# Performance work log

Hardware: AMD Instinct MI355X
Metric: run time of the kernel (lower is better)

Reference implementation:

```python
import jax, jax.numpy as jnp
import numpy as np

N, K, D, P, H, DH = 8192, 32, 256, 64, 8, 32
NBATCH, NCHAIN, RBF_BINS = 32, 64, 16


def _normalize(v, eps=1e-8):
    return v / jnp.sqrt((v * v).sum(-1, keepdims=True) + eps)


def _rbf(d, d_min, d_max, n):
    centers = jnp.linspace(d_min, d_max, n)
    sigma = (d_max - d_min) / n
    return jnp.exp(-(((d[..., None] - centers) / sigma) ** 2))


def _ln(x, g, b, eps=1e-5):
    m = x.mean(-1, keepdims=True)
    v = ((x - m) ** 2).mean(-1, keepdims=True)
    return (x - m) * jax.lax.rsqrt(v + eps) * g + b


def _frames(pos):
    # backbone frame from N (atom 0), CA (atom 1), C (atom 2)
    n, ca, c = pos[:, 0], pos[:, 1], pos[:, 2]
    e1 = _normalize(c - ca)
    u = n - ca
    e2 = _normalize(u - (u * e1).sum(-1, keepdims=True) * e1)
    e3 = jnp.cross(e1, e2)
    return jnp.stack([e1, e2, e3], axis=-1), ca  # R [N,3,3] (columns), t [N,3]


def setup_inputs():
    key = jax.random.key(0)
    ks = iter(jax.random.split(key, 64))

    def nrm(shape, scale=1.0):
        return (jax.random.normal(next(ks), shape) * scale).astype(jnp.float32)

    def lin(i, o):
        return nrm((i, o), 1.0 / np.sqrt(i))

    inp = {}
    inp['local'] = nrm((N, D))
    inp['pos'] = nrm((N, 5, 3), 3.0)
    inp['neighbours'] = jax.random.randint(next(ks), (N, K), 0, N)
    inp['resi'] = jnp.arange(N)
    inp['chain'] = jnp.sort(jax.random.randint(next(ks), (N,), 0, NCHAIN))
    inp['batch'] = jnp.sort(jax.random.randint(next(ks), (N,), 0, NBATCH))
    inp['mask'] = jnp.ones((N,), dtype=bool)
    # pair feature projections
    inp['w_relpos'] = lin(65, P)
    inp['w_dist'] = lin(RBF_BINS, P)
    inp['w_dir'] = lin(15, P)
    inp['w_rot'] = lin(12, P)
    inp['ln_pair_g'] = jnp.ones((P,)); inp['ln_pair_b'] = jnp.zeros((P,))
    inp['w_p1'] = lin(P, 2 * P); inp['b_p1'] = jnp.zeros((2 * P,))
    inp['w_p2'] = lin(2 * P, P); inp['b_p2'] = jnp.zeros((P,))
    # sparse structure attention
    inp['wq'] = lin(D, H * DH); inp['wk'] = lin(D, H * DH); inp['wv'] = lin(D, H * DH)
    inp['wb'] = lin(P, H)
    inp['wo'] = lin(H * DH, D)
    inp['ln_a_g'] = jnp.ones((D,)); inp['ln_a_b'] = jnp.zeros((D,))
    # update block
    inp['w_t1'] = lin(K * (RBF_BINS + 3), 2 * D)
    inp['w_t2'] = lin(2 * D, D)
    inp['w_up'] = lin(D, 2 * D)
    inp['w_lg'] = lin(D, 2 * D); inp['w_cg'] = lin(D, 2 * D); inp['w_bg'] = lin(D, 2 * D)
    inp['w_out'] = lin(2 * D, D); inp['b_out'] = jnp.zeros((D,))
    inp['ln_u_g'] = jnp.ones((D,)); inp['ln_u_b'] = jnp.zeros((D,))
    inp['ln_f_g'] = jnp.ones((D,)); inp['ln_f_b'] = jnp.zeros((D,))
    return inp


def reference(local, pos, neighbours, resi, chain, batch, mask,
              w_relpos, w_dist, w_dir, w_rot, ln_pair_g, ln_pair_b,
              w_p1, b_p1, w_p2, b_p2,
              wq, wk, wv, wb, wo, ln_a_g, ln_a_b,
              w_t1, w_t2, w_up, w_lg, w_cg, w_bg, w_out, b_out,
              ln_u_g, ln_u_b, ln_f_g, ln_f_b):
    mask_f = mask.astype(jnp.float32)
    valid = (neighbours >= 0).astype(jnp.float32)
    pair_mask = mask_f[:, None] * mask_f[neighbours] * valid  # [N,K]

    # ---- pair features: relpos + distance + direction + rotation ----
    same_chain = (chain[neighbours] == chain[:, None]).astype(jnp.float32)
    off = jnp.clip(resi[neighbours] - resi[:, None], -32, 32) + 32
    relpos = jax.nn.one_hot(off, 65, dtype=jnp.float32) * same_chain[..., None]
    pair = relpos @ w_relpos                                  # [N,K,P]

    cb = pos[:, 4]
    d_cb = jnp.sqrt(((cb[neighbours] - cb[:, None]) ** 2).sum(-1) + 1e-8)
    pair += _rbf(d_cb, 0.0, 22.0, RBF_BINS) @ w_dist

    ca = pos[:, 1]
    dirs = _normalize(pos[neighbours] - ca[:, None, None])    # [N,K,5,3]
    pair += dirs.reshape(N, K, 15) @ w_dir

    R, t = _frames(pos)
    Rn = R[neighbours]                                        # [N,K,3,3]
    rel_R = jnp.einsum('nab,nkac->nkbc', R, Rn).reshape(N, K, 9)
    rel_t = jnp.einsum('nab,nka->nkb', R, t[neighbours] - t[:, None])
    pair += jnp.concatenate([rel_R, rel_t], -1) @ w_rot

    pair = _ln(pair, ln_pair_g, ln_pair_b)
    pair = jax.nn.gelu(pair @ w_p1 + b_p1) @ w_p2 + b_p2      # MLP 2P -> P

    # ---- resi-dual streams ----
    x, inc = local, local

    # ---- sparse structure attention over neighbour set ----
    q = (x @ wq).reshape(N, H, DH)
    k = (x @ wk)[neighbours].reshape(N, K, H, DH)
    v = (x @ wv)[neighbours].reshape(N, K, H, DH)
    logits = jnp.einsum('nhd,nkhd->nhk', q, k) / np.sqrt(DH).astype(np.float32)
    logits += (pair @ wb).transpose(0, 2, 1)                  # pair bias [N,H,K]
    logits = jnp.where(pair_mask[:, None, :] > 0, logits, -1e9)
    attn = jax.nn.softmax(logits, axis=-1)
    o = jnp.einsum('nhk,nkhd->nhd', attn, v).reshape(N, H * DH)
    y = (o @ wo) * mask_f[:, None]
    x = _ln(x + y, ln_a_g, ln_a_b)
    inc = inc + y

    # ---- global/chain gated update with scatter-mean (index_mean) ----
    rel_ca = jnp.einsum('nab,nka->nkb', R, ca[neighbours] - ca[:, None])  # local frame [N,K,3]
    d_rel = jnp.sqrt((rel_ca ** 2).sum(-1) + 1e-8)
    tfeat = jnp.concatenate([_rbf(d_rel, 0.0, 22.0, RBF_BINS), _normalize(rel_ca)], -1)
    tfeat = (tfeat * pair_mask[..., None]).reshape(N, K * (RBF_BINS + 3))
    tfeat = (jax.nn.gelu(tfeat @ w_t1) @ w_t2) * mask_f[:, None]

    up = x @ w_up
    lg = jax.nn.gelu(x @ w_lg)
    cg = jax.nn.gelu(x @ w_cg)
    bg = jax.nn.gelu(x @ w_bg)

    def index_mean(val, idx, nseg):
        m = mask_f[:, None]
        s = jax.ops.segment_sum(val * m, idx, num_segments=nseg)
        c = jax.ops.segment_sum(m, idx, num_segments=nseg)
        return (s / jnp.maximum(c, 1.0))[idx]

    hidden = bg * index_mean(up, batch, NBATCH) + cg * index_mean(up, chain, NCHAIN) + lg * up
    y2 = hidden @ w_out + b_out + tfeat
    x = _ln(x + y2, ln_u_g, ln_u_b)
    inc = inc + y2

    # resi-dual finisher: x + LayerNorm(incremental)
    return x + _ln(inc, ln_f_g, ln_f_b)
```

## Files before the change

### kernel.cpp

```cpp
#include <hip/hip_runtime.h>
#include <math.h>

#define NN 8192
#define KK 32
#define DD 256
#define PP 64
#define HH 8
#define DHH 32
#define NBATCH 32
#define NCHAIN 64

typedef __attribute__((ext_vector_type(8))) short bf16x8;
typedef __attribute__((ext_vector_type(4))) float f32x4;

__device__ __forceinline__ float gelu_f(float x) {
    float x3 = x * x * x;
    float e = __expf(fmaf(x3, -0.07135481f, x * -1.59576912f));
    return __fdividef(x, 1.f + e);
}

__device__ __forceinline__ float wave_sum64(float v) {
    #pragma unroll
    for (int m = 32; m > 0; m >>= 1) v += __shfl_xor(v, m);
    return v;
}

__device__ __forceinline__ ushort f2bf(float x) {
    union { float f; unsigned int u; } v; v.f = x;
    unsigned int r = v.u + 0x7fffu + ((v.u >> 16) & 1u);
    return (ushort)(r >> 16);
}

__device__ __forceinline__ float bf2f(ushort u) {
    union { unsigned int u; float f; } v; v.u = ((unsigned int)u) << 16;
    return v.f;
}

__device__ __forceinline__ uint pk2(float a, float b) {
    return (uint)f2bf(a) | ((uint)f2bf(b) << 16);
}

__global__ __launch_bounds__(256) void frames_kernel(const float* __restrict__ pos,
                                                     float* __restrict__ R) {
    int n = blockIdx.x * 256 + threadIdx.x;
    if (n >= NN) return;
    const float* p = pos + n * 15;
    float nx = p[0], ny = p[1], nz = p[2];
    float cax = p[3], cay = p[4], caz = p[5];
    float cx = p[6], cy = p[7], cz = p[8];
    float e1x = cx - cax, e1y = cy - cay, e1z = cz - caz;
    float inv = rsqrtf(e1x * e1x + e1y * e1y + e1z * e1z + 1e-8f);
    e1x *= inv; e1y *= inv; e1z *= inv;
    float ux = nx - cax, uy = ny - cay, uz = nz - caz;
    float dt = ux * e1x + uy * e1y + uz * e1z;
    float e2x = ux - dt * e1x, e2y = uy - dt * e1y, e2z = uz - dt * e1z;
    inv = rsqrtf(e2x * e2x + e2y * e2y + e2z * e2z + 1e-8f);
    e2x *= inv; e2y *= inv; e2z *= inv;
    float e3x = e1y * e2z - e1z * e2y;
    float e3y = e1z * e2x - e1x * e2z;
    float e3z = e1x * e2y - e1y * e2x;
    float* r = R + n * 9;
    r[0] = e1x; r[1] = e2x; r[2] = e3x;
    r[3] = e1y; r[4] = e2y; r[5] = e3y;
    r[6] = e1z; r[7] = e2z; r[8] = e3z;
}

__global__ __launch_bounds__(256) void pair_raw_kernel(
    const float* __restrict__ pos, const int* __restrict__ nbr,
    const int* __restrict__ resi, const int* __restrict__ chain,
    const float* __restrict__ R,
    ushort* __restrict__ feat, int* __restrict__ relidx, float* __restrict__ tfeat_raw) {
    int p = blockIdx.x * 256 + threadIdx.x;
    int n = p >> 5, k = p & 31;
    int j = nbr[p];
    int same = (chain[j] == chain[n]);
    int off = min(max(resi[j] - resi[n], -32), 32) + 32;
    relidx[p] = same ? off : -1;

    float can0 = pos[n * 15 + 3], can1 = pos[n * 15 + 4], can2 = pos[n * 15 + 5];
    float cbn0 = pos[n * 15 + 12], cbn1 = pos[n * 15 + 13], cbn2 = pos[n * 15 + 14];
    float Rn[9], Rj[9];
    #pragma unroll
    for (int i = 0; i < 9; i++) Rn[i] = R[n * 9 + i];
    #pragma unroll
    for (int i = 0; i < 9; i++) Rj[i] = R[j * 9 + i];
    float pj[15];
    #pragma unroll
    for (int i = 0; i < 15; i++) pj[i] = pos[j * 15 + i];

    float fe[43];
    float d0 = pj[12] - cbn0, d1 = pj[13] - cbn1, d2 = pj[14] - cbn2;
    float dcb = sqrtf(d0 * d0 + d1 * d1 + d2 * d2 + 1e-8f);
    #pragma unroll
    for (int i = 0; i < 16; i++) {
        float c = (22.f / 15.f) * (float)i;
        float z = (dcb - c) * (1.f / 1.375f);
        fe[i] = __expf(-z * z);
    }
    #pragma unroll
    for (int a = 0; a < 5; a++) {
        float vx = pj[a * 3 + 0] - can0;
        float vy = pj[a * 3 + 1] - can1;
        float vz = pj[a * 3 + 2] - can2;
        float invv = rsqrtf(vx * vx + vy * vy + vz * vz + 1e-8f);
        fe[16 + a * 3 + 0] = vx * invv;
        fe[16 + a * 3 + 1] = vy * invv;
        fe[16 + a * 3 + 2] = vz * invv;
    }
    #pragma unroll
    for (int b = 0; b < 3; b++)
        #pragma unroll
        for (int c2 = 0; c2 < 3; c2++)
            fe[31 + b * 3 + c2] = Rn[0 + b] * Rj[0 + c2] + Rn[3 + b] * Rj[3 + c2] + Rn[6 + b] * Rj[6 + c2];
    float t0 = pj[3] - can0, t1 = pj[4] - can1, t2 = pj[5] - can2;
    #pragma unroll
    for (int b = 0; b < 3; b++)
        fe[40 + b] = Rn[0 + b] * t0 + Rn[3 + b] * t1 + Rn[6 + b] * t2;

    #pragma unroll
    for (int q = 0; q < 8; q++) {
        uint4 w;
        float v0 = (q * 8 + 0 < 43) ? fe[q * 8 + 0] : 0.f;
        float v1 = (q * 8 + 1 < 43) ? fe[q * 8 + 1] : 0.f;
        float v2 = (q * 8 + 2 < 43) ? fe[q * 8 + 2] : 0.f;
        float v3 = (q * 8 + 3 < 43) ? fe[q * 8 + 3] : 0.f;
        float v4 = (q * 8 + 4 < 43) ? fe[q * 8 + 4] : 0.f;
        float v5 = (q * 8 + 5 < 43) ? fe[q * 8 + 5] : 0.f;
        float v6 = (q * 8 + 6 < 43) ? fe[q * 8 + 6] : 0.f;
        float v7 = (q * 8 + 7 < 43) ? fe[q * 8 + 7] : 0.f;
        w.x = pk2(v0, v1); w.y = pk2(v2, v3); w.z = pk2(v4, v5); w.w = pk2(v6, v7);
        *(uint4*)&feat[(size_t)p * 64 + q * 8] = w;
    }
    float rt0 = fe[40], rt1 = fe[41], rt2 = fe[42];
    float dr2 = rt0 * rt0 + rt1 * rt1 + rt2 * rt2 + 1e-8f;
    float invdr = rsqrtf(dr2);
    float drel = dr2 * invdr;
    float* tf = tfeat_raw + (size_t)n * 608 + k * 19;
    #pragma unroll
    for (int i = 0; i < 16; i++) {
        float c = (22.f / 15.f) * (float)i;
        float z = (drel - c) * (1.f / 1.375f);
        tf[i] = __expf(-z * z);
    }
    tf[16] = rt0 * invdr;
    tf[17] = rt1 * invdr;
    tf[18] = rt2 * invdr;
}

__global__ __launch_bounds__(256) void w2b_kernel(
    const float* __restrict__ w_p2, const float* __restrict__ b_p2,
    const float* __restrict__ wb, float* __restrict__ w2b, float* __restrict__ b2b) {
    int idx = blockIdx.x * 256 + threadIdx.x;
    if (idx < 1024) {
        int c = idx >> 3, h = idx & 7;
        float s = 0.f;
        for (int q = 0; q < 64; q++) s += w_p2[c * 64 + q] * wb[q * 8 + h];
        w2b[idx] = s;
    }
    if (idx < 8) {
        float s = 0.f;
        for (int q = 0; q < 64; q++) s += b_p2[q] * wb[q * 8 + idx];
        b2b[idx] = s;
    }
}

__global__ __launch_bounds__(256) void fmt_kernel(
    const float* __restrict__ w_p1,
    const float* __restrict__ w_dist, const float* __restrict__ w_dir,
    const float* __restrict__ w_rot, const float* __restrict__ w2b,
    ushort* __restrict__ pf) {
    int u = blockIdx.x * 256 + threadIdx.x;
    uint* pfu = (uint*)pf;
    if (u < 4096) {
        int fs = u >> 8, rem = u & 255, lane = rem >> 2, jj = rem & 3;
        int hi = lane >> 4, lo = lane & 15;
        int f = fs >> 1, s = fs & 1;
        int k0 = 32 * s + hi * 8 + 2 * jj;
        int c = 16 * f + lo;
        pfu[u] = pk2(w_p1[k0 * 128 + c], w_p1[(k0 + 1) * 128 + c]);
    } else if (u < 5120) {
        int u2 = u - 4096;
        int s2 = u2 >> 8, rem = u2 & 255, lane = rem >> 2, jj = rem & 3;
        int hi = lane >> 4, lo = lane & 15;
        int c0 = 32 * s2 + 8 * hi + 2 * jj;
        float v0 = (lo < 8) ? w2b[c0 * 8 + lo] : 0.f;
        float v1 = (lo < 8) ? w2b[(c0 + 1) * 8 + lo] : 0.f;
        pfu[u] = pk2(v0, v1);
    } else if (u < 7168) {
        int u2 = u - 5120;
        int fs = u2 >> 8, rem = u2 & 255, lane = rem >> 2, jj = rem & 3;
        int hi = lane >> 4, lo = lane & 15;
        int f = fs >> 1, s = fs & 1;
        int k0 = 32 * s + hi * 8 + 2 * jj;
        int c = 16 * f + lo;
        float v0 = (k0 < 16) ? w_dist[k0 * 64 + c] : (k0 < 31) ? w_dir[(k0 - 16) * 64 + c]
                 : (k0 < 43) ? w_rot[(k0 - 31) * 64 + c] : 0.f;
        int k1 = k0 + 1;
        float v1 = (k1 < 16) ? w_dist[k1 * 64 + c] : (k1 < 31) ? w_dir[(k1 - 16) * 64 + c]
                 : (k1 < 43) ? w_rot[(k1 - 31) * 64 + c] : 0.f;
        pfu[u] = pk2(v0, v1);
    }
}

__global__ __launch_bounds__(256) void pair_pre_kernel(
    ushort* feat, const int* __restrict__ relidx,
    const float* __restrict__ w_relpos, const ushort* __restrict__ pf,
    const float* __restrict__ lng, const float* __restrict__ lnb) {
    int tid = threadIdx.x;
    int wid = tid >> 6, lane = tid & 63, hi = lane >> 4, lo = lane & 15;
    bf16x8 wf[8];
    #pragma unroll
    for (int fs = 0; fs < 8; fs++) wf[fs] = *(const bf16x8*)&pf[10240 + fs * 512 + lane * 8];
    float sg_r[4][4], sbt_r[4][4];
    #pragma unroll
    for (int f = 0; f < 4; f++)
        #pragma unroll
        for (int r = 0; r < 4; r++) {
            int c = 16 * f + 4 * hi + r;
            sg_r[f][r] = lng[c];
            sbt_r[f][r] = lnb[c];
        }
    const f32x4 zz = {0.f, 0.f, 0.f, 0.f};
    for (int t = blockIdx.x * 4 + wid; t < (NN * KK / 16); t += 16384) {
        int r0 = t << 4;
        bf16x8 bp0 = *(const bf16x8*)(feat + (size_t)(r0 + lo) * 64 + hi * 8);
        bf16x8 bp1 = *(const bf16x8*)(feat + (size_t)(r0 + lo) * 64 + 32 + hi * 8);
        f32x4 a0f[4];
        #pragma unroll
        for (int f = 0; f < 4; f++) {
            a0f[f] = __builtin_amdgcn_mfma_f32_16x16x32_bf16(wf[f * 2 + 0], bp0, zz, 0, 0, 0);
            a0f[f] = __builtin_amdgcn_mfma_f32_16x16x32_bf16(wf[f * 2 + 1], bp1, a0f[f], 0, 0, 0);
        }
        int ridx = relidx[r0 + lo];
        float val[4][4];
        float part = 0.f;
        #pragma unroll
        for (int f = 0; f < 4; f++)
            #pragma unroll
            for (int r = 0; r < 4; r++) {
                int c = 16 * f + 4 * hi + r;
                float rv = (ridx >= 0) ? w_relpos[ridx * 64 + c] : 0.f;
                float v = a0f[f][r] + rv;
                val[f][r] = v;
                part += v;
            }
        part += __shfl_xor(part, 16);
        part += __shfl_xor(part, 32);
        float mean = part * (1.f / 64.f);
        float v2 = 0.f;
        #pragma unroll
        for (int f = 0; f < 4; f++)
            #pragma unroll
            for (int r = 0; r < 4; r++) {
                float dv = val[f][r] - mean;
                val[f][r] = dv;
                v2 += dv * dv;
// ... 19 lines not shown
    float* __restrict__ bias) {
    __shared__ __align__(16) ushort hx[4 * 2048];
    int tid = threadIdx.x;
    int wid = tid >> 6, lane = tid & 63, hi = lane >> 4, lo = lane & 15;
    bf16x8 w1f[16];
    #pragma unroll
    for (int fs = 0; fs < 16; fs++) w1f[fs] = *(const bf16x8*)&pf[fs * 512 + lane * 8];
    bf16x8 w2f[4];
    #pragma unroll
    for (int s2 = 0; s2 < 4; s2++) w2f[s2] = *(const bf16x8*)&pf[8192 + s2 * 512 + lane * 8];
    float b2b_r[4];
    #pragma unroll
    for (int r = 0; r < 4; r++) b2b_r[r] = (hi < 2) ? b2b[4 * hi + r] : 0.f;
    float sb1_r[8][4];
    #pragma unroll
    for (int f = 0; f < 8; f++)
        #pragma unroll
        for (int r = 0; r < 4; r++) sb1_r[f][r] = b_p1[16 * f + 4 * hi + r];

    ushort* hxw = &hx[wid * 2048];
    const f32x4 zz = {0.f, 0.f, 0.f, 0.f};
    for (int t = blockIdx.x * 4 + wid; t < (NN * KK / 16); t += 16384) {
        int r0 = t << 4;
        bf16x8 bh0 = *(const bf16x8*)(pln + (size_t)(r0 + lo) * 64 + hi * 8);
        bf16x8 bh1 = *(const bf16x8*)(pln + (size_t)(r0 + lo) * 64 + 32 + hi * 8);
        #pragma unroll
        for (int f = 0; f < 8; f++) {
            f32x4 acch = __builtin_amdgcn_mfma_f32_16x16x32_bf16(w1f[f * 2 + 0], bh0, zz, 0, 0, 0);
            acch = __builtin_amdgcn_mfma_f32_16x16x32_bf16(w1f[f * 2 + 1], bh1, acch, 0, 0, 0);
            int c0 = 16 * f + 4 * hi;
            float v0 = gelu_f(acch[0] + sb1_r[f][0]);
            float v1 = gelu_f(acch[1] + sb1_r[f][1]);
            float v2b = gelu_f(acch[2] + sb1_r[f][2]);
            float v3 = gelu_f(acch[3] + sb1_r[f][3]);
            int idx = (lo * 128 + c0) ^ ((lo & 7) << 3);
            *(uint2*)&hxw[idx] = make_uint2(pk2(v0, v1), pk2(v2b, v3));
        }
        f32x4 acc = zz;
        #pragma unroll
        for (int s2 = 0; s2 < 4; s2++) {
            int idx = (lo * 128 + 32 * s2 + 8 * hi) ^ ((lo & 7) << 3);
            bf16x8 bh = *(const bf16x8*)&hxw[idx];
            acc = __builtin_amdgcn_mfma_f32_16x16x32_bf16(w2f[s2], bh, acc, 0, 0, 0);
        }
        if (hi < 2) {
            int n = r0 >> 5, kb = (r0 & 31) + lo;
            #pragma unroll
            for (int r = 0; r < 4; r++)
                bias[(size_t)n * 256 + (4 * hi + r) * 32 + kb] = acc[r] + b2b_r[r];
        }
    }
}

__device__ __forceinline__ void gemm_core(
    const float* __restrict__ A, const float* __restrict__ W,
    int K, int WN, int row0, int colW0, int tid,
    ushort* sA, ushort* sB, f32x4 acc[4][4]) {
    int wid = tid >> 6, lane = tid & 63, lo = lane & 15, hi = lane >> 4;
    int wr = wid >> 1, wc = wid & 1;
    int ar = tid >> 1, akh = (tid & 1) * 16;
    int bcol = tid & 127, bks = (tid >> 7) * 16;
    for (int kt = 0; kt < K; kt += 32) {
        const float* ap = &A[(size_t)(row0 + ar) * K + kt + akh];
        float4 a0 = *(const float4*)(ap + 0);
        float4 a1 = *(const float4*)(ap + 4);
        float4 a2 = *(const float4*)(ap + 8);
        float4 a3 = *(const float4*)(ap + 12);
        float wv[16];
        #pragma unroll
        for (int i = 0; i < 16; i++) wv[i] = W[(size_t)(kt + bks + i) * WN + colW0 + bcol];
        __syncthreads();
        *(uint4*)&sA[ar * 40 + akh] = make_uint4(pk2(a0.x, a0.y), pk2(a0.z, a0.w), pk2(a1.x, a1.y), pk2(a1.z, a1.w));
        *(uint4*)&sA[ar * 40 + akh + 8] = make_uint4(pk2(a2.x, a2.y), pk2(a2.z, a2.w), pk2(a3.x, a3.y), pk2(a3.z, a3.w));
        *(uint4*)&sB[bcol * 40 + bks] = make_uint4(pk2(wv[0], wv[1]), pk2(wv[2], wv[3]), pk2(wv[4], wv[5]), pk2(wv[6], wv[7]));
        *(uint4*)&sB[bcol * 40 + bks + 8] = make_uint4(pk2(wv[8], wv[9]), pk2(wv[10], wv[11]), pk2(wv[12], wv[13]), pk2(wv[14], wv[15]));
        __syncthreads();
        bf16x8 af[4], bfr[4];
        #pragma unroll
        for (int mi = 0; mi < 4; mi++) af[mi] = *(const bf16x8*)&sA[(wr * 64 + mi * 16 + lo) * 40 + hi * 8];
        #pragma unroll
        for (int ni = 0; ni < 4; ni++) bfr[ni] = *(const bf16x8*)&sB[(wc * 64 + ni * 16 + lo) * 40 + hi * 8];
        #pragma unroll
        for (int mi = 0; mi < 4; mi++)
            #pragma unroll
            for (int ni = 0; ni < 4; ni++)
                acc[mi][ni] = __builtin_amdgcn_mfma_f32_16x16x32_bf16(af[mi], bfr[ni], acc[mi][ni], 0, 0, 0);
    }
}

__global__ __launch_bounds__(256) void gemm_t1(
    const float* __restrict__ A, const float* __restrict__ W, ushort* __restrict__ C,
    int M, int K, int Nc) {
    __shared__ __align__(16) ushort sA[128 * 40];
    __shared__ __align__(16) ushort sB[128 * 40];
    int row0 = blockIdx.y * 128, col0 = blockIdx.x * 128;
    int tid = threadIdx.x;
    const f32x4 zz = {0.f, 0.f, 0.f, 0.f};
    f32x4 acc[4][4] = {{zz, zz, zz, zz}, {zz, zz, zz, zz}, {zz, zz, zz, zz}, {zz, zz, zz, zz}};
    gemm_core(A, W, K, Nc, row0, col0, tid, sA, sB, acc);
    int wid = tid >> 6, lane = tid & 63, lo = lane & 15, hi = lane >> 4;
    int wr = wid >> 1, wc = wid & 1;
    #pragma unroll
    for (int ni = 0; ni < 4; ni++) {
        int col = col0 + wc * 64 + ni * 16 + lo;
        #pragma unroll
        for (int mi = 0; mi < 4; mi++) {
            #pragma unroll
            for (int r = 0; r < 4; r++) {
                int row = row0 + wr * 64 + mi * 16 + hi * 4 + r;
                C[(size_t)row * Nc + col] = f2bf(gelu_f(acc[mi][ni][r]));
            }
        }
    }
}

__global__ __launch_bounds__(256) void gemm_n64b(
    const ushort* __restrict__ A, const float* __restrict__ W, float* __restrict__ C,
    int M, int K, int Nc,
    const float* __restrict__ bias, const float* __restrict__ addp) {
    __shared__ __align__(16) ushort sA[128 * 40];
    __shared__ __align__(16) ushort sB[64 * 40];
    int row0 = blockIdx.y * 128, col0 = blockIdx.x * 64;
    int tid = threadIdx.x;
    int wid = tid >> 6, lane = tid & 63, lo = lane & 15, hi = lane >> 4;
    int wr = wid >> 1, wc = wid & 1;
    int ar = tid >> 1, akh = (tid & 1) * 16;
    int bcol = tid & 63, bks = (tid >> 6) * 8;
    const f32x4 zz = {0.f, 0.f, 0.f, 0.f};
    f32x4 acc[4][2] = {{zz, zz}, {zz, zz}, {zz, zz}, {zz, zz}};
    for (int kt = 0; kt < K; kt += 32) {
        const ushort* ap = &A[(size_t)(row0 + ar) * K + kt + akh];
        uint4 a01 = *(const uint4*)(ap);
        uint4 a23 = *(const uint4*)(ap + 8);
        float wv[8];
        #pragma unroll
        for (int i = 0; i < 8; i++) wv[i] = W[(size_t)(kt + bks + i) * Nc + col0 + bcol];
        __syncthreads();
        *(uint4*)&sA[ar * 40 + akh] = a01;
        *(uint4*)&sA[ar * 40 + akh + 8] = a23;
        *(uint2*)&sB[bcol * 40 + bks] = make_uint2(pk2(wv[0], wv[1]), pk2(wv[2], wv[3]));
        *(uint2*)&sB[bcol * 40 + bks + 4] = make_uint2(pk2(wv[4], wv[5]), pk2(wv[6], wv[7]));
        __syncthreads();
        bf16x8 af[4], bfr[2];
        #pragma unroll
        for (int mi = 0; mi < 4; mi++) af[mi] = *(const bf16x8*)&sA[(wr * 64 + mi * 16 + lo) * 40 + hi * 8];
        #pragma unroll
        for (int ni = 0; ni < 2; ni++) bfr[ni] = *(const bf16x8*)&sB[(wc * 32 + ni * 16 + lo) * 40 + hi * 8];
        #pragma unroll
        for (int mi = 0; mi < 4; mi++)
            #pragma unroll
            for (int ni = 0; ni < 2; ni++)
                acc[mi][ni] = __builtin_amdgcn_mfma_f32_16x16x32_bf16(af[mi], bfr[ni], acc[mi][ni], 0, 0, 0);
    }
    #pragma unroll
    for (int ni = 0; ni < 2; ni++) {
        int col = col0 + wc * 32 + ni * 16 + lo;
        float bc = bias ? bias[col] : 0.f;
        #pragma unroll
        for (int mi = 0; mi < 4; mi++) {
            #pragma unroll
            for (int r = 0; r < 4; r++) {
                int row = row0 + wr * 64 + mi * 16 + hi * 4 + r;
                float v = acc[mi][ni][r] + bc;
                if (addp) v += addp[(size_t)row * Nc + col];
                C[(size_t)row * Nc + col] = v;
            }
        }
    }
}

__global__ __launch_bounds__(256) void gemm_qkv(
    const float* __restrict__ A, const float* __restrict__ wq, const float* __restrict__ wk,
    const float* __restrict__ wvp, float* __restrict__ qb, ushort* __restrict__ kb,
    ushort* __restrict__ vb, int K) {
    __shared__ __align__(16) ushort sA[128 * 40];
    __shared__ __align__(16) ushort sB[128 * 40];
    int row0 = blockIdx.y * 128, col0 = blockIdx.x * 128;
    int wsel = col0 >> 8, colW0 = col0 & 255;
    const float* W = (wsel == 0) ? wq : (wsel == 1) ? wk : wvp;
    int tid = threadIdx.x;
    const f32x4 zz = {0.f, 0.f, 0.f, 0.f};
    f32x4 acc[4][4] = {{zz, zz, zz, zz}, {zz, zz, zz, zz}, {zz, zz, zz, zz}, {zz, zz, zz, zz}};
    gemm_core(A, W, K, 256, row0, colW0, tid, sA, sB, acc);
    int wid = tid >> 6, lane = tid & 63, lo = lane & 15, hi = lane >> 4;
    int wr = wid >> 1, wc = wid & 1;
    #pragma unroll
    for (int ni = 0; ni < 4; ni++) {
        int colW = colW0 + wc * 64 + ni * 16 + lo;
        #pragma unroll
        for (int mi = 0; mi < 4; mi++) {
            #pragma unroll
            for (int r = 0; r < 4; r++) {
                int row = row0 + wr * 64 + mi * 16 + hi * 4 + r;
                float v = acc[mi][ni][r];
                if (wsel == 0) qb[(size_t)row * 256 + colW] = v;
                else if (wsel == 1) kb[(size_t)row * 256 + colW] = f2bf(v);
                else vb[(size_t)row * 256 + colW] = f2bf(v);
            }
        }
    }
}

__global__ __launch_bounds__(256) void gemm_ffn(
    const float* __restrict__ A,
    const float* __restrict__ w0, const float* __restrict__ w1,
    const float* __restrict__ w2, const float* __restrict__ w3,
    ushort* __restrict__ o0, ushort* __restrict__ o1,
    ushort* __restrict__ o2, ushort* __restrict__ o3, int K) {
    __shared__ __align__(16) ushort sA[128 * 40];
    __shared__ __align__(16) ushort sB[128 * 40];
    int row0 = blockIdx.y * 128, col0 = blockIdx.x * 128;
    int wsel = col0 >> 9, colW0 = col0 & 511;
    const float* W = (wsel == 0) ? w0 : (wsel == 1) ? w1 : (wsel == 2) ? w2 : w3;
    ushort* O = (wsel == 0) ? o0 : (wsel == 1) ? o1 : (wsel == 2) ? o2 : o3;
    int tid = threadIdx.x;
    const f32x4 zz = {0.f, 0.f, 0.f, 0.f};
    f32x4 acc[4][4] = {{zz, zz, zz, zz}, {zz, zz, zz, zz}, {zz, zz, zz, zz}, {zz, zz, zz, zz}};
    gemm_core(A, W, K, 512, row0, colW0, tid, sA, sB, acc);
    int wid = tid >> 6, lane = tid & 63, lo = lane & 15, hi = lane >> 4;
    int wr = wid >> 1, wc = wid & 1;
    #pragma unroll
    for (int ni = 0; ni < 4; ni++) {
        int colW = colW0 + wc * 64 + ni * 16 + lo;
        #pragma unroll
        for (int mi = 0; mi < 4; mi++) {
            #pragma unroll
            for (int r = 0; r < 4; r++) {
                int row = row0 + wr * 64 + mi * 16 + hi * 4 + r;
                float v = acc[mi][ni][r];
                if (wsel > 0) v = gelu_f(v);
                O[(size_t)row * 512 + colW] = f2bf(v);
            }
        }
    }
}

__global__ __launch_bounds__(256) void attn_kernel(
    const float* __restrict__ q, const ushort* __restrict__ kp, const ushort* __restrict__ vp,
    const float* __restrict__ bias, const int* __restrict__ nbr, ushort* __restrict__ o) {
    int n = blockIdx.x;
    __shared__ float qs[256];
    __shared__ int js[32];
    __shared__ float ls[256];
    __shared__ __align__(16) uint4 vs[32 * 33];
    int t = threadIdx.x;
    qs[t] = q[(size_t)n * 256 + t];
    if (t < 32) js[t] = nbr[n * 32 + t];
    __syncthreads();
    int vrow = t >> 3, vseg = t & 7;
    const uint4* vsrc = (const uint4*)(vp + (size_t)js[vrow] * 256);
    uint4 vr0 = vsrc[vseg * 4 + 0];
    uint4 vr1 = vsrc[vseg * 4 + 1];
    uint4 vr2 = vsrc[vseg * 4 + 2];
    uint4 vr3 = vsrc[vseg * 4 + 3];
    int h = t >> 5, k = t & 31;
    int j = js[k];
    const bf16x8* kr = (const bf16x8*)(kp + (size_t)j * 256 + h * 32);
    bf16x8 kv0 = kr[0], kv1 = kr[1], kv2 = kr[2], kv3 = kr[3];
    const float* qh = qs + h * 32;
    float dot = 0.f;
    #pragma unroll
    for (int i = 0; i < 8; i++) dot += qh[i] * bf2f((ushort)kv0[i]);
    #pragma unroll
    for (int i = 0; i < 8; i++) dot += qh[8 + i] * bf2f((ushort)kv1[i]);
    #pragma unroll
    for (int i = 0; i < 8; i++) dot += qh[16 + i] * bf2f((ushort)kv2[i]);
    #pragma unroll
    for (int i = 0; i < 8; i++) dot += qh[24 + i] * bf2f((ushort)kv3[i]);
    float l = dot * 0.17677669529663687f + bias[(size_t)n * 256 + t];
    float mx = l;
    #pragma unroll
    for (int m = 16; m > 0; m >>= 1) mx = fmaxf(mx, __shfl_xor(mx, m));
    float e = __expf(l - mx);
    float sum = e;
    #pragma unroll
    for (int m = 16; m > 0; m >>= 1) sum += __shfl_xor(sum, m);
    ls[t] = e / sum;
    vs[vrow * 33 + vseg * 4 + 0] = vr0;
    vs[vrow * 33 + vseg * 4 + 1] = vr1;
    vs[vrow * 33 + vseg * 4 + 2] = vr2;
    vs[vrow * 33 + vseg * 4 + 3] = vr3;
    __syncthreads();
    const ushort* vsu = (const ushort*)vs;
    const float* lh = ls + h * 32;
    float acc = 0.f;
    #pragma unroll
    for (int kk = 0; kk < 32; kk++)
        acc += lh[kk] * bf2f(vsu[kk * 264 + h * 32 + k]);
    o[(size_t)n * 256 + t] = f2bf(acc);
}

__global__ __launch_bounds__(256) void ln_add_kernel(
    const float* __restrict__ a, const float* __restrict__ b,
    const float* __restrict__ g, const float* __restrict__ be,
    float* __restrict__ xout, float* __restrict__ sout) {
    int row = blockIdx.x * 4 + (threadIdx.x >> 6);
    int lane = threadIdx.x & 63;
    size_t base = (size_t)row * 256 + lane * 4;
    float4 av = *(const float4*)(a + base);
    float4 bv = *(const float4*)(b + base);
    float s0 = av.x + bv.x, s1 = av.y + bv.y, s2 = av.z + bv.z, s3 = av.w + bv.w;
    float sum = wave_sum64(s0 + s1 + s2 + s3);
    float mean = sum * (1.f / 256.f);
    float d0 = s0 - mean, d1 = s1 - mean, d2 = s2 - mean, d3 = s3 - mean;
    float v = wave_sum64(d0 * d0 + d1 * d1 + d2 * d2 + d3 * d3);
    float rs = rsqrtf(v * (1.f / 256.f) + 1e-5f);
    float4 gv = *(const float4*)(g + lane * 4);
    float4 bev = *(const float4*)(be + lane * 4);
    float4 xo;
    xo.x = d0 * rs * gv.x + bev.x;
    xo.y = d1 * rs * gv.y + bev.y;
    xo.z = d2 * rs * gv.z + bev.z;
    xo.w = d3 * rs * gv.w + bev.w;
    *(float4*)(xout + base) = xo;
    float4 so; so.x = s0; so.y = s1; so.z = s2; so.w = s3;
    *(float4*)(sout + base) = so;
}

__global__ __launch_bounds__(256) void seg_partial_kernel(
    const ushort* __restrict__ up, const int* __restrict__ batch, const int* __restrict__ chain,
    float* __restrict__ mb_acc, float* __restrict__ mc_acc) {
    int r0 = blockIdx.x * 32;
    int t = threadIdx.x;
    float ab0 = 0.f, ab1 = 0.f, ac0 = 0.f, ac1 = 0.f;
    int curb = batch[r0], curc = chain[r0];
    for (int r = r0; r < r0 + 32; r++) {
        int b = batch[r], c = chain[r];
        if (b != curb) {
            atomicAdd(&mb_acc[curb * 512 + t], ab0);
            atomicAdd(&mb_acc[curb * 512 + 256 + t], ab1);
            ab0 = ab1 = 0.f; curb = b;
        }
        if (c != curc) {
            atomicAdd(&mc_acc[curc * 512 + t], ac0);
            atomicAdd(&mc_acc[curc * 512 + 256 + t], ac1);
            ac0 = ac1 = 0.f; curc = c;
        }
        float v0 = bf2f(up[(size_t)r * 512 + t]);
        float v1 = bf2f(up[(size_t)r * 512 + 256 + t]);
        ab0 += v0; ab1 += v1; ac0 += v0; ac1 += v1;
    }
    atomicAdd(&mb_acc[curb * 512 + t], ab0);
    atomicAdd(&mb_acc[curb * 512 + 256 + t], ab1);
    atomicAdd(&mc_acc[curc * 512 + t], ac0);
    atomicAdd(&mc_acc[curc * 512 + 256 + t], ac1);
}

__device__ __forceinline__ int lower_bound_i(const int* a, int n, int v) {
    int lo = 0, hi = n;
    while (lo < hi) { int mid = (lo + hi) >> 1; if (a[mid] < v) lo = mid + 1; else hi = mid; }
    return lo;
}

__global__ __launch_bounds__(256) void seg_final_kernel(
    float* __restrict__ mb, float* __restrict__ mc,
    const int* __restrict__ batch, const int* __restrict__ chain) {
    int idx = blockIdx.x * 256 + threadIdx.x;
    if (idx < NBATCH * 512) {
        int seg = idx >> 9;
        int lo = lower_bound_i(batch, NN, seg);
        int hi = lower_bound_i(batch, NN, seg + 1);
        mb[idx] *= 1.f / fmaxf((float)(hi - lo), 1.f);
    } else {
        int i2 = idx - NBATCH * 512;
        int seg = i2 >> 9;
        int lo = lower_bound_i(chain, NN, seg);
        int hi = lower_bound_i(chain, NN, seg + 1);
// ... 55 lines not shown
    ov.y = (sd1 * rss * ugv.y + ubv.y) + (td1 * rst * fgv.y + fbv.y);
    ov.z = (sd2 * rss * ugv.z + ubv.z) + (td2 * rst * fgv.z + fbv.z);
    ov.w = (sd3 * rss * ugv.w + ubv.w) + (td3 * rst * fgv.w + fbv.w);
    *(float4*)(out + base) = ov;
}

extern "C" void kernel_launch(void* const* d_in, const int* in_sizes, int n_in,
                              void* d_out, int out_size, void* d_ws, size_t ws_size,
                              hipStream_t stream) {
    const float* local    = (const float*)d_in[0];
    const float* pos      = (const float*)d_in[1];
    const int*   nbr      = (const int*)d_in[2];
    const int*   resi     = (const int*)d_in[3];
    const int*   chain    = (const int*)d_in[4];
    const int*   batch    = (const int*)d_in[5];
    const float* w_relpos = (const float*)d_in[7];
    const float* w_dist   = (const float*)d_in[8];
    const float* w_dir    = (const float*)d_in[9];
    const float* w_rot    = (const float*)d_in[10];
    const float* ln_pair_g = (const float*)d_in[11];
    const float* ln_pair_b = (const float*)d_in[12];
    const float* w_p1     = (const float*)d_in[13];
    const float* b_p1     = (const float*)d_in[14];
    const float* w_p2     = (const float*)d_in[15];
    const float* b_p2     = (const float*)d_in[16];
    const float* wq       = (const float*)d_in[17];
    const float* wk       = (const float*)d_in[18];
    const float* wv       = (const float*)d_in[19];
    const float* wb       = (const float*)d_in[20];
    const float* wo       = (const float*)d_in[21];
    const float* ln_a_g   = (const float*)d_in[22];
    const float* ln_a_b   = (const float*)d_in[23];
    const float* w_t1     = (const float*)d_in[24];
    const float* w_t2     = (const float*)d_in[25];
    const float* w_up     = (const float*)d_in[26];
    const float* w_lg     = (const float*)d_in[27];
    const float* w_cg     = (const float*)d_in[28];
    const float* w_bg     = (const float*)d_in[29];
    const float* w_out    = (const float*)d_in[30];
    const float* b_out    = (const float*)d_in[31];
    const float* ln_u_g   = (const float*)d_in[32];
    const float* ln_u_b   = (const float*)d_in[33];
    const float* ln_f_g   = (const float*)d_in[34];
    const float* ln_f_b   = (const float*)d_in[35];

    float* ws = (float*)d_ws;
    float* R         = ws + 0;
    float* biasb     = ws + 73728;
    float* tfeat_out = ws + 2170880;
    float* x1        = ws + 4268032;
    float* inc1      = ws + 6365184;
    ushort* featb    = (ushort*)(ws + 8462336);
    int* relidx      = (int*)(ws + 16850944);
    float* tfeat_raw = ws + 17113088;
    ushort* pfmt     = (ushort*)(ws + 22093824);
    ushort* tmp512u  = (ushort*)(ws + 22101824);
    float* qb        = ws + 8462336;
    ushort* kbu      = (ushort*)(ws + 10559488);
    ushort* vbu      = (ushort*)(ws + 12656640);
    ushort* obu      = (ushort*)(ws + 14753792);
    float* yb        = ws + 24199232;
    ushort* upbu     = (ushort*)(ws + 8462336);
    ushort* lgbu     = (ushort*)(ws + 12656640);
    ushort* cgbu     = (ushort*)(ws + 17113088);
    ushort* bgbu     = (ushort*)(ws + 21307392);
    float* mb        = ws + 26296384;
    float* mc        = ws + 26312768;
    float* y2        = ws + 26345536;
    float* w2b       = ws + 26296384;
    float* b2b       = ws + 26297408;

    frames_kernel<<<NN / 256, 256, 0, stream>>>(pos, R);
    w2b_kernel<<<4, 256, 0, stream>>>(w_p2, b_p2, wb, w2b, b2b);
    fmt_kernel<<<28, 256, 0, stream>>>(w_p1, w_dist, w_dir, w_rot, w2b, pfmt);
    pair_raw_kernel<<<NN * KK / 256, 256, 0, stream>>>(pos, nbr, resi, chain, R,
                                                       featb, relidx, tfeat_raw);
    pair_pre_kernel<<<4096, 256, 0, stream>>>(featb, relidx, w_relpos, pfmt,
                                              ln_pair_g, ln_pair_b);
    pair_mlp2_kernel<<<4096, 256, 0, stream>>>(featb, pfmt, b_p1, b2b, biasb);
    gemm_t1<<<dim3(4, 64), 256, 0, stream>>>(tfeat_raw, w_t1, tmp512u, NN, 608, 512);
    gemm_n64b<<<dim3(4, 64), 256, 0, stream>>>(tmp512u, w_t2, tfeat_out, NN, 512, 256, nullptr, nullptr);
    gemm_qkv<<<dim3(6, 64), 256, 0, stream>>>(local, wq, wk, wv, qb, kbu, vbu, 256);
    attn_kernel<<<NN, 256, 0, stream>>>(qb, kbu, vbu, biasb, nbr, obu);
    gemm_n64b<<<dim3(4, 64), 256, 0, stream>>>(obu, wo, yb, NN, 256, 256, nullptr, nullptr);
    ln_add_kernel<<<NN / 4, 256, 0, stream>>>(local, yb, ln_a_g, ln_a_b, x1, inc1);
    gemm_ffn<<<dim3(16, 64), 256, 0, stream>>>(x1, w_up, w_lg, w_cg, w_bg,
                                               upbu, lgbu, cgbu, bgbu, 256);
    (void)hipMemsetAsync(mb, 0, (NBATCH + NCHAIN) * 512 * sizeof(float), stream);
    seg_partial_kernel<<<NN / 32, 256, 0, stream>>>(upbu, batch, chain, mb, mc);
    seg_final_kernel<<<(NBATCH + NCHAIN) * 512 / 256, 256, 0, stream>>>(mb, mc, batch, chain);
    hidden_kernel<<<NN * 512 / 1024, 256, 0, stream>>>(upbu, cgbu, bgbu, lgbu, mb, mc, batch, chain);
    gemm_n64b<<<dim3(4, 64), 256, 0, stream>>>(lgbu, w_out, y2, NN, 512, 256, b_out, tfeat_out);
    final_kernel<<<NN / 4, 256, 0, stream>>>(x1, y2, inc1, ln_u_g, ln_u_b, ln_f_g, ln_f_b, (float*)d_out);
}
```

Baseline: 294.5 us.

## Pre-transpose weights to bf16 and feed GEMMs bf16 activations

Adds a kernel that converts every dense weight matrix to a transposed bf16 layout once per call. The GEMM cores can then load B tiles as contiguous 16-byte vectors instead of strided scalar fp32 loads with per-element packing. Activations feeding the GEMMs (tfeat, local, x1) are also produced or converted as bf16, which halves their read traffic and removes conversion work from the GEMM loops. The cost is two extra launches (weight transpose, local conversion), a reshuffled workspace, and some extra bf16 rounding of tfeat features.

```diff
diff --git a/kernel.cpp b/kernel.cpp
--- a/kernel.cpp
+++ b/kernel.cpp
@@ -69,7 +69,7 @@
     const float* __restrict__ pos, const int* __restrict__ nbr,
     const int* __restrict__ resi, const int* __restrict__ chain,
     const float* __restrict__ R,
-    ushort* __restrict__ feat, int* __restrict__ relidx, float* __restrict__ tfeat_raw) {
+    ushort* __restrict__ feat, int* __restrict__ relidx, ushort* __restrict__ tfb) {
     int p = blockIdx.x * 256 + threadIdx.x;
     int n = p >> 5, k = p & 31;
     int j = nbr[p];
@@ -135,16 +135,16 @@
     float dr2 = rt0 * rt0 + rt1 * rt1 + rt2 * rt2 + 1e-8f;
     float invdr = rsqrtf(dr2);
     float drel = dr2 * invdr;
-    float* tf = tfeat_raw + (size_t)n * 608 + k * 19;
+    ushort* tf = tfb + (size_t)n * 608 + k * 19;
     #pragma unroll
     for (int i = 0; i < 16; i++) {
         float c = (22.f / 15.f) * (float)i;
         float z = (drel - c) * (1.f / 1.375f);
-        tf[i] = __expf(-z * z);
-    }
-    tf[16] = rt0 * invdr;
-    tf[17] = rt1 * invdr;
-    tf[18] = rt2 * invdr;
+        tf[i] = f2bf(__expf(-z * z));
+    }
+    tf[16] = f2bf(rt0 * invdr);
+    tf[17] = f2bf(rt1 * invdr);
+    tf[18] = f2bf(rt2 * invdr);
 }
 
 __global__ __launch_bounds__(256) void w2b_kernel(
@@ -202,6 +202,48 @@
     }
 }
 
+__global__ __launch_bounds__(256) void fmt_wt_kernel(
+    const float* __restrict__ w0, const float* __restrict__ w1,
+    const float* __restrict__ w2, const float* __restrict__ w3,
+    const float* __restrict__ w4, const float* __restrict__ w5,
+    const float* __restrict__ w6, const float* __restrict__ w7,
+    const float* __restrict__ w8, const float* __restrict__ w9,
+    const float* __restrict__ w10, ushort* __restrict__ wt) {
+    __shared__ ushort tile[32][33];
+    int z = blockIdx.z;
+    const float* W; int K, N; size_t off;
+    switch (z) {
+        case 0:  W = w0;  K = 256; N = 512; off = 0;       break;
+        case 1:  W = w1;  K = 256; N = 512; off = 131072;  break;
+        case 2:  W = w2;  K = 256; N = 512; off = 262144;  break;
+        case 3:  W = w3;  K = 256; N = 512; off = 393216;  break;
+        case 4:  W = w4;  K = 256; N = 256; off = 524288;  break;
+        case 5:  W = w5;  K = 256; N = 256; off = 589824;  break;
+        case 6:  W = w6;  K = 256; N = 256; off = 655360;  break;
+        case 7:  W = w7;  K = 608; N = 512; off = 720896;  break;
+        case 8:  W = w8;  K = 512; N = 256; off = 1032192; break;
+        case 9:  W = w9;  K = 256; N = 256; off = 1163264; break;
+        default: W = w10; K = 512; N = 256; off = 1228800; break;
+    }
+    int bk = blockIdx.y * 32, bn = blockIdx.x * 32;
+    if (bk >= K || bn >= N) return;
+    int tx = threadIdx.x & 31, ty = threadIdx.x >> 5;
+    #pragma unroll
+    for (int i = 0; i < 32; i += 8)
+        tile[ty + i][tx] = f2bf(W[(size_t)(bk + ty + i) * N + bn + tx]);
+    __syncthreads();
+    #pragma unroll
+    for (int i = 0; i < 32; i += 8)
+        wt[off + (size_t)(bn + ty + i) * K + bk + tx] = tile[tx][ty + i];
+}
+
+__global__ __launch_bounds__(256) void convb_kernel(const float* __restrict__ src,
+                                                    ushort* __restrict__ dst) {
+    size_t i4 = ((size_t)blockIdx.x * 256 + threadIdx.x) * 4;
+    float4 v = *(const float4*)&src[i4];
+    *(uint2*)&dst[i4] = make_uint2(pk2(v.x, v.y), pk2(v.z, v.w));
+}
+
 __global__ __launch_bounds__(256) void pair_pre_kernel(
     ushort* feat, const int* __restrict__ relidx,
     const float* __restrict__ w_relpos, const ushort* __restrict__ pf,
@@ -327,28 +369,25 @@
     }
 }
 
-__device__ __forceinline__ void gemm_core(
-    const float* __restrict__ A, const float* __restrict__ W,
-    int K, int WN, int row0, int colW0, int tid,
+__device__ __forceinline__ void gemm_coreT(
+    const ushort* __restrict__ A, const ushort* __restrict__ Wt,
+    int K, int row0, int colW0, int tid,
     ushort* sA, ushort* sB, f32x4 acc[4][4]) {
     int wid = tid >> 6, lane = tid & 63, lo = lane & 15, hi = lane >> 4;
     int wr = wid >> 1, wc = wid & 1;
     int ar = tid >> 1, akh = (tid & 1) * 16;
-    int bcol = tid & 127, bks = (tid >> 7) * 16;
     for (int kt = 0; kt < K; kt += 32) {
-        const float* ap = &A[(size_t)(row0 + ar) * K + kt + akh];
-        float4 a0 = *(const float4*)(ap + 0);
-        float4 a1 = *(const float4*)(ap + 4);
-        float4 a2 = *(const float4*)(ap + 8);
-        float4 a3 = *(const float4*)(ap + 12);
-        float wv[16];
-        #pragma unroll
-        for (int i = 0; i < 16; i++) wv[i] = W[(size_t)(kt + bks + i) * WN + colW0 + bcol];
+        const ushort* ap = &A[(size_t)(row0 + ar) * K + kt + akh];
+        uint4 a01 = *(const uint4*)ap;
+        uint4 a23 = *(const uint4*)(ap + 8);
+        const ushort* bp = &Wt[(size_t)(colW0 + ar) * K + kt + akh];
+        uint4 b01 = *(const uint4*)bp;
+        uint4 b23 = *(const uint4*)(bp + 8);
         __syncthreads();
-        *(uint4*)&sA[ar * 40 + akh] = make_uint4(pk2(a0.x, a0.y), pk2(a0.z, a0.w), pk2(a1.x, a1.y), pk2(a1.z, a1.w));
-        *(uint4*)&sA[ar * 40 + akh + 8] = make_uint4(pk2(a2.x, a2.y), pk2(a2.z, a2.w), pk2(a3.x, a3.y), pk2(a3.z, a3.w));
-        *(uint4*)&sB[bcol * 40 + bks] = make_uint4(pk2(wv[0], wv[1]), pk2(wv[2], wv[3]), pk2(wv[4], wv[5]), pk2(wv[6], wv[7]));
-        *(uint4*)&sB[bcol * 40 + bks + 8] = make_uint4(pk2(wv[8], wv[9]), pk2(wv[10], wv[11]), pk2(wv[12], wv[13]), pk2(wv[14], wv[15]));
+        *(uint4*)&sA[ar * 40 + akh] = a01;
+        *(uint4*)&sA[ar * 40 + akh + 8] = a23;
+        *(uint4*)&sB[ar * 40 + akh] = b01;
+        *(uint4*)&sB[ar * 40 + akh + 8] = b23;
         __syncthreads();
         bf16x8 af[4], bfr[4];
         #pragma unroll
@@ -363,16 +402,16 @@
     }
 }
 
-__global__ __launch_bounds__(256) void gemm_t1(
-    const float* __restrict__ A, const float* __restrict__ W, ushort* __restrict__ C,
-    int M, int K, int Nc) {
+__global__ __launch_bounds__(256) void gemm_t1T(
+    const ushort* __restrict__ A, const ushort* __restrict__ Wt, ushort* __restrict__ C,
+    int K, int Nc) {
     __shared__ __align__(16) ushort sA[128 * 40];
     __shared__ __align__(16) ushort sB[128 * 40];
     int row0 = blockIdx.y * 128, col0 = blockIdx.x * 128;
     int tid = threadIdx.x;
     const f32x4 zz = {0.f, 0.f, 0.f, 0.f};
     f32x4 acc[4][4] = {{zz, zz, zz, zz}, {zz, zz, zz, zz}, {zz, zz, zz, zz}, {zz, zz, zz, zz}};
-    gemm_core(A, W, K, Nc, row0, col0, tid, sA, sB, acc);
+    gemm_coreT(A, Wt, K, row0, col0, tid, sA, sB, acc);
     int wid = tid >> 6, lane = tid & 63, lo = lane & 15, hi = lane >> 4;
     int wr = wid >> 1, wc = wid & 1;
     #pragma unroll
@@ -389,10 +428,9 @@
     }
 }
 
-__global__ __launch_bounds__(256) void gemm_n64b(
-    const ushort* __restrict__ A, const float* __restrict__ W, float* __restrict__ C,
-    int M, int K, int Nc,
-    const float* __restrict__ bias, const float* __restrict__ addp) {
+__global__ __launch_bounds__(256) void gemm_n64T(
+    const ushort* __restrict__ A, const ushort* __restrict__ Wt, float* __restrict__ C,
+    int K, int Nc, const float* __restrict__ bias, const float* __restrict__ addp) {
     __shared__ __align__(16) ushort sA[128 * 40];
     __shared__ __align__(16) ushort sB[64 * 40];
     int row0 = blockIdx.y * 128, col0 = blockIdx.x * 64;
@@ -400,21 +438,18 @@
     int wid = tid >> 6, lane = tid & 63, lo = lane & 15, hi = lane >> 4;
     int wr = wid >> 1, wc = wid & 1;
     int ar = tid >> 1, akh = (tid & 1) * 16;
-    int bcol = tid & 63, bks = (tid >> 6) * 8;
+    int br = tid >> 2, bkh = (tid & 3) * 8;
     const f32x4 zz = {0.f, 0.f, 0.f, 0.f};
     f32x4 acc[4][2] = {{zz, zz}, {zz, zz}, {zz, zz}, {zz, zz}};
     for (int kt = 0; kt < K; kt += 32) {
         const ushort* ap = &A[(size_t)(row0 + ar) * K + kt + akh];
-        uint4 a01 = *(const uint4*)(ap);
+        uint4 a01 = *(const uint4*)ap;
         uint4 a23 = *(const uint4*)(ap + 8);
-        float wv[8];
-        #pragma unroll
-        for (int i = 0; i < 8; i++) wv[i] = W[(size_t)(kt + bks + i) * Nc + col0 + bcol];
+        uint4 b0 = *(const uint4*)&Wt[(size_t)(col0 + br) * K + kt + bkh];
         __syncthreads();
         *(uint4*)&sA[ar * 40 + akh] = a01;
         *(uint4*)&sA[ar * 40 + akh + 8] = a23;
-        *(uint2*)&sB[bcol * 40 + bks] = make_uint2(pk2(wv[0], wv[1]), pk2(wv[2], wv[3]));
-        *(uint2*)&sB[bcol * 40 + bks + 4] = make_uint2(pk2(wv[4], wv[5]), pk2(wv[6], wv[7]));
+        *(uint4*)&sB[br * 40 + bkh] = b0;
         __syncthreads();
         bf16x8 af[4], bfr[2];
         #pragma unroll
@@ -444,59 +479,54 @@
     }
 }
 
-__global__ __launch_bounds__(256) void gemm_qkv(
-    const float* __restrict__ A, const float* __restrict__ wq, const float* __restrict__ wk,
-    const float* __restrict__ wvp, float* __restrict__ qb, ushort* __restrict__ kb,
-    ushort* __restrict__ vb, int K) {
+__global__ __launch_bounds__(256) void gemm_qkvT(
+    const ushort* __restrict__ A, const ushort* __restrict__ Wt3,
+    float* __restrict__ qb, ushort* __restrict__ kb, ushort* __restrict__ vb) {
     __shared__ __align__(16) ushort sA[128 * 40];
     __shared__ __align__(16) ushort sB[128 * 40];
     int row0 = blockIdx.y * 128, col0 = blockIdx.x * 128;
-    int wsel = col0 >> 8, colW0 = col0 & 255;
-    const float* W = (wsel == 0) ? wq : (wsel == 1) ? wk : wvp;
+    int wsel = col0 >> 8, colW = col0 & 255;
     int tid = threadIdx.x;
     const f32x4 zz = {0.f, 0.f, 0.f, 0.f};
     f32x4 acc[4][4] = {{zz, zz, zz, zz}, {zz, zz, zz, zz}, {zz, zz, zz, zz}, {zz, zz, zz, zz}};
-    gemm_core(A, W, K, 256, row0, colW0, tid, sA, sB, acc);
+    gemm_coreT(A, Wt3, 256, row0, col0, tid, sA, sB, acc);
     int wid = tid >> 6, lane = tid & 63, lo = lane & 15, hi = lane >> 4;
     int wr = wid >> 1, wc = wid & 1;
     #pragma unroll
     for (int ni = 0; ni < 4; ni++) {
-        int colW = colW0 + wc * 64 + ni * 16 + lo;
+        int colo = colW + wc * 64 + ni * 16 + lo;
         #pragma unroll
         for (int mi = 0; mi < 4; mi++) {
             #pragma unroll
             for (int r = 0; r < 4; r++) {
                 int row = row0 + wr * 64 + mi * 16 + hi * 4 + r;
                 float v = acc[mi][ni][r];
-                if (wsel == 0) qb[(size_t)row * 256 + colW] = v;
-                else if (wsel == 1) kb[(size_t)row * 256 + colW] = f2bf(v);
-                else vb[(size_t)row * 256 + colW] = f2bf(v);
+                if (wsel == 0) qb[(size_t)row * 256 + colo] = v;
+                else if (wsel == 1) kb[(size_t)row * 256 + colo] = f2bf(v);
+                else vb[(size_t)row * 256 + colo] = f2bf(v);
             }
         }
     }
 }
 
-__global__ __launch_bounds__(256) void gemm_ffn(
-    const float* __restrict__ A,
-    const float* __restrict__ w0, const float* __restrict__ w1,
-    const float* __restrict__ w2, const float* __restrict__ w3,
+__global__ __launch_bounds__(256) void gemm_ffnT(
+    const ushort* __restrict__ A, const ushort* __restrict__ Wt4,
     ushort* __restrict__ o0, ushort* __restrict__ o1,
-    ushort* __restrict__ o2, ushort* __restrict__ o3, int K) {
+    ushort* __restrict__ o2, ushort* __restrict__ o3) {
     __shared__ __align__(16) ushort sA[128 * 40];
     __shared__ __align__(16) ushort sB[128 * 40];
     int row0 = blockIdx.y * 128, col0 = blockIdx.x * 128;
-    int wsel = col0 >> 9, colW0 = col0 & 511;
-    const float* W = (wsel == 0) ? w0 : (wsel == 1) ? w1 : (wsel == 2) ? w2 : w3;
+    int wsel = col0 >> 9, colW = col0 & 511;
     ushort* O = (wsel == 0) ? o0 : (wsel == 1) ? o1 : (wsel == 2) ? o2 : o3;
     int tid = threadIdx.x;
     const f32x4 zz = {0.f, 0.f, 0.f, 0.f};
     f32x4 acc[4][4] = {{zz, zz, zz, zz}, {zz, zz, zz, zz}, {zz, zz, zz, zz}, {zz, zz, zz, zz}};
-    gemm_core(A, W, K, 512, row0, colW0, tid, sA, sB, acc);
+    gemm_coreT(A, Wt4, 256, row0, col0, tid, sA, sB, acc);
     int wid = tid >> 6, lane = tid & 63, lo = lane & 15, hi = lane >> 4;
     int wr = wid >> 1, wc = wid & 1;
     #pragma unroll
     for (int ni = 0; ni < 4; ni++) {
-        int colW = colW0 + wc * 64 + ni * 16 + lo;
+        int colo = colW + wc * 64 + ni * 16 + lo;
         #pragma unroll
         for (int mi = 0; mi < 4; mi++) {
             #pragma unroll
@@ -504,7 +534,7 @@
                 int row = row0 + wr * 64 + mi * 16 + hi * 4 + r;
                 float v = acc[mi][ni][r];
                 if (wsel > 0) v = gelu_f(v);
-                O[(size_t)row * 512 + colW] = f2bf(v);
+                O[(size_t)row * 512 + colo] = f2bf(v);
             }
         }
     }
@@ -568,7 +598,7 @@
 __global__ __launch_bounds__(256) void ln_add_kernel(
     const float* __restrict__ a, const float* __restrict__ b,
     const float* __restrict__ g, const float* __restrict__ be,
-    float* __restrict__ xout, float* __restrict__ sout) {
+    float* __restrict__ xout, ushort* __restrict__ xbout, float* __restrict__ sout) {
     int row = blockIdx.x * 4 + (threadIdx.x >> 6);
     int lane = threadIdx.x & 63;
     size_t base = (size_t)row * 256 + lane * 4;
@@ -588,6 +618,7 @@
     xo.z = d2 * rs * gv.z + bev.z;
     xo.w = d3 * rs * gv.w + bev.w;
     *(float4*)(xout + base) = xo;
+    *(uint2*)(xbout + base) = make_uint2(pk2(xo.x, xo.y), pk2(xo.z, xo.w));
     float4 so; so.x = s0; so.y = s1; so.z = s2; so.w = s3;
     *(float4*)(sout + base) = so;
 }
@@ -749,44 +780,52 @@
     float* inc1      = ws + 6365184;
     ushort* featb    = (ushort*)(ws + 8462336);
     int* relidx      = (int*)(ws + 16850944);
-    float* tfeat_raw = ws + 17113088;
-    ushort* pfmt     = (ushort*)(ws + 22093824);
-    ushort* tmp512u  = (ushort*)(ws + 22101824);
+    ushort* tfb      = (ushort*)(ws + 17113088);
+    ushort* wt       = (ushort*)(ws + 19603456);
+    ushort* x1b      = (ushort*)(ws + 20283392);
+    ushort* localb   = (ushort*)(ws + 21331968);
+    ushort* tmp512u  = (ushort*)(ws + 22380544);
+    float* y2        = ws + 22380544;
+    float* yb        = ws + 17113088;
     float* qb        = ws + 8462336;
     ushort* kbu      = (ushort*)(ws + 10559488);
-    ushort* vbu      = (ushort*)(ws + 12656640);
-    ushort* obu      = (ushort*)(ws + 14753792);
-    float* yb        = ws + 24199232;
+    ushort* vbu      = (ushort*)(ws + 11608064);
+    ushort* obu      = (ushort*)(ws + 12656640);
     ushort* upbu     = (ushort*)(ws + 8462336);
-    ushort* lgbu     = (ushort*)(ws + 12656640);
-    ushort* cgbu     = (ushort*)(ws + 17113088);
-    ushort* bgbu     = (ushort*)(ws + 21307392);
-    float* mb        = ws + 26296384;
-    float* mc        = ws + 26312768;
-    float* y2        = ws + 26345536;
-    float* w2b       = ws + 26296384;
-    float* b2b       = ws + 26297408;
+    ushort* lgbu     = (ushort*)(ws + 10559488);
+    ushort* cgbu     = (ushort*)(ws + 12656640);
+    ushort* bgbu     = (ushort*)(ws + 14753792);
+    float* mb        = ws + 24477696;
+    float* mc        = ws + 24494080;
+    ushort* pfmt     = (ushort*)(ws + 24526848);
+    float* w2b       = ws + 24534016;
+    float* b2b       = ws + 24535040;
 
     frames_kernel<<<NN / 256, 256, 0, stream>>>(pos, R);
     w2b_kernel<<<4, 256, 0, stream>>>(w_p2, b_p2, wb, w2b, b2b);
     fmt_kernel<<<28, 256, 0, stream>>>(w_p1, w_dist, w_dir, w_rot, w2b, pfmt);
+    fmt_wt_kernel<<<dim3(16, 19, 11), 256, 0, stream>>>(w_up, w_lg, w_cg, w_bg, wq, wk, wv,
+                                                        w_t1, w_t2, wo, w_out, wt);
+    convb_kernel<<<NN * 256 / 1024, 256, 0, stream>>>(local, localb);
     pair_raw_kernel<<<NN * KK / 256, 256, 0, stream>>>(pos, nbr, resi, chain, R,
-                                                       featb, relidx, tfeat_raw);
+                                                       featb, relidx, tfb);
     pair_pre_kernel<<<4096, 256, 0, stream>>>(featb, relidx, w_relpos, pfmt,
                                               ln_pair_g, ln_pair_b);
     pair_mlp2_kernel<<<4096, 256, 0, stream>>>(featb, pfmt, b_p1, b2b, biasb);
-    gemm_t1<<<dim3(4, 64), 256, 0, stream>>>(tfeat_raw, w_t1, tmp512u, NN, 608, 512);
-    gemm_n64b<<<dim3(4, 64), 256, 0, stream>>>(tmp512u, w_t2, tfeat_out, NN, 512, 256, nullptr, nullptr);
-    gemm_qkv<<<dim3(6, 64), 256, 0, stream>>>(local, wq, wk, wv, qb, kbu, vbu, 256);
+    gemm_t1T<<<dim3(4, 64), 256, 0, stream>>>(tfb, wt + 720896, tmp512u, 608, 512);
+    gemm_n64T<<<dim3(4, 64), 256, 0, stream>>>(tmp512u, wt + 1032192, tfeat_out, 512, 256,
+                                               nullptr, nullptr);
+    gemm_qkvT<<<dim3(6, 64), 256, 0, stream>>>(localb, wt + 524288, qb, kbu, vbu);
     attn_kernel<<<NN, 256, 0, stream>>>(qb, kbu, vbu, biasb, nbr, obu);
-    gemm_n64b<<<dim3(4, 64), 256, 0, stream>>>(obu, wo, yb, NN, 256, 256, nullptr, nullptr);
-    ln_add_kernel<<<NN / 4, 256, 0, stream>>>(local, yb, ln_a_g, ln_a_b, x1, inc1);
-    gemm_ffn<<<dim3(16, 64), 256, 0, stream>>>(x1, w_up, w_lg, w_cg, w_bg,
-                                               upbu, lgbu, cgbu, bgbu, 256);
+    gemm_n64T<<<dim3(4, 64), 256, 0, stream>>>(obu, wt + 1163264, yb, 256, 256,
+                                               nullptr, nullptr);
+    ln_add_kernel<<<NN / 4, 256, 0, stream>>>(local, yb, ln_a_g, ln_a_b, x1, x1b, inc1);
+    gemm_ffnT<<<dim3(16, 64), 256, 0, stream>>>(x1b, wt, upbu, lgbu, cgbu, bgbu);
     (void)hipMemsetAsync(mb, 0, (NBATCH + NCHAIN) * 512 * sizeof(float), stream);
     seg_partial_kernel<<<NN / 32, 256, 0, stream>>>(upbu, batch, chain, mb, mc);
     seg_final_kernel<<<(NBATCH + NCHAIN) * 512 / 256, 256, 0, stream>>>(mb, mc, batch, chain);
     hidden_kernel<<<NN * 512 / 1024, 256, 0, stream>>>(upbu, cgbu, bgbu, lgbu, mb, mc, batch, chain);
-    gemm_n64b<<<dim3(4, 64), 256, 0, stream>>>(lgbu, w_out, y2, NN, 512, 256, b_out, tfeat_out);
+    gemm_n64T<<<dim3(4, 64), 256, 0, stream>>>(lgbu, wt + 1228800, y2, 512, 256,
+                                               b_out, tfeat_out);
     final_kernel<<<NN / 4, 256, 0, stream>>>(x1, y2, inc1, ln_u_g, ln_u_b, ln_f_g, ln_f_b, (float*)d_out);
 }
```

New measurement: 269.3 us. 8.6% less time.
